# Performance work log

Hardware: AMD Instinct MI355X
Metric: run time of the kernel (lower is better)

The kernel has to match this reference:

```python
import jax, jax.numpy as jnp
import numpy as np

B, T, N1, K = 128, 512, 512, 8   # batch, steps, n_customers+1, knn_k
CAPACITY = 50.0
NEG_INF = -1e9


def setup_inputs() -> dict:
    key = jax.random.key(0)
    k0, k1, k2, k3, k4, k5 = jax.random.split(key, 6)
    psi_prime = jax.random.normal(k0, (B, N1, 2), dtype=jnp.float32)
    demands = jax.random.uniform(k1, (B, N1), dtype=jnp.float32) * 9.0 + 1.0
    demands = demands.at[:, 0].set(0.0)  # depot has zero demand
    actions = jax.random.randint(k2, (B, T), 0, N1, dtype=jnp.int32)
    knn_indices = jax.random.randint(k3, (B, N1, K), 0, N1, dtype=jnp.int32)
    Wq_w = jax.random.normal(k4, (2, 4), dtype=jnp.float32) * 0.5
    Wq_b = jax.random.normal(k5, (2,), dtype=jnp.float32) * 0.1
    lambda_param = jnp.float32(0.1)
    return {"psi_prime": psi_prime, "demands": demands, "Wq_w": Wq_w,
            "Wq_b": Wq_b, "lambda_param": lambda_param,
            "actions": actions, "knn_indices": knn_indices}


def _rollout_states(demands, actions):
    """Reconstruct the T per-step states (cur, used, vis) BEFORE each action."""
    mb, Tn = actions.shape
    n1 = demands.shape[1]
    batch = jnp.arange(mb)

    def step(carry, act_t):
        cur, used, vis = carry
        out = (cur, used, vis)  # record state before applying act_t
        at_depot = act_t == 0
        dem_t = jnp.take_along_axis(demands, act_t[:, None], axis=1)[:, 0]
        used_n = jnp.where(at_depot, 0.0, used + dem_t)
        vis_n = vis.at[batch, act_t].set(True)
        vis_n = vis_n.at[:, 0].set(False)
        return (act_t, used_n, vis_n), out

    init = (jnp.zeros((mb,), jnp.int32), jnp.zeros((mb,), jnp.float32),
            jnp.zeros((mb, n1), dtype=bool))
    _, (all_cur, all_used, all_vis) = jax.lax.scan(step, init, actions.T)
    # scan stacks over leading T axis -> move batch first
    return all_cur.T, all_used.T, jnp.transpose(all_vis, (1, 0, 2))


def _evaluate(psi_prime, demands, Wq_w, Wq_b, lambda_param, actions, knn_indices):
    mb, Tn = actions.shape
    n_cust = psi_prime.shape[1] - 1

    all_cur, all_used, all_vis = _rollout_states(demands, actions)  # [B,T],[B,T],[B,T,N1]

    remaining = CAPACITY - all_used                      # [B,T]
    cap_norm = remaining / max(CAPACITY, 1e-8)
    exceeds = demands[:, None, :] > remaining[:, :, None]  # [B,T,N1]
    mask = all_vis | exceeds
    mask = mask.at[:, :, 0].set(False)
    at_depot = all_cur == 0                               # [B,T]
    has_cust = jnp.any(~mask[:, :, 1:], axis=-1)
    mask = mask.at[:, :, 0].set(at_depot & has_cust)

    psi_curr = jnp.take_along_axis(psi_prime, all_cur[:, :, None], axis=1)  # [B,T,2]
    psi_curr = jnp.where(at_depot[:, :, None], 0.0, psi_curr)
    t_norm = jnp.arange(Tn, dtype=jnp.float32) / max(n_cust, 1)
    t_norm = jnp.broadcast_to(t_norm[None, :], (mb, Tn))
    ctx = jnp.concatenate([psi_curr, cap_norm[:, :, None], t_norm[:, :, None]], axis=-1)  # [B,T,4]

    query = ctx @ Wq_w.T + Wq_b                           # [B,T,2]
    context_scores = jnp.einsum('btd,bnd->btn', query, psi_prime)  # [B,T,N1]

    # kNN interference: per-node dot with its k nearest neighbours, summed
    neigh = psi_prime[jnp.arange(mb)[:, None, None], knn_indices]  # [B,N1,K,2]
    interf = jnp.einsum('bnd,bnkd->bn', psi_prime, neigh)          # [B,N1]

    scores = context_scores + lambda_param * interf[:, None, :]
    scores = jnp.where(mask, NEG_INF, scores)
    log_probs = jax.nn.log_softmax(scores, axis=-1)                # [B,T,N1]

    lp_new = jnp.take_along_axis(log_probs, actions[:, :, None], axis=2)[:, :, 0]  # [B,T]
    ent = -jnp.sum(jnp.exp(log_probs) * log_probs, axis=-1)        # [B,T]
    entropy = ent.mean(axis=1)                                     # [B]
    return lp_new, entropy


def reference(psi_prime, demands, Wq_w, Wq_b, lambda_param, actions, knn_indices):
    return _evaluate(psi_prime, demands, Wq_w, Wq_b, lambda_param, actions, knn_indices)
```

## Files before the change

kernel.cpp:

```cpp
#include <hip/hip_runtime.h>
#include <hip/hip_bf16.h>

#define B_  128
#define T_  512
#define N1_ 512
#define K_  8
#define CAPf 50.0f
#define NEG_INF_F (-1000000000.0f)

__device__ __forceinline__ int   fi(float x) { return __float_as_int(x); }
__device__ __forceinline__ float uf(int x)   { return __int_as_float(x); }

__device__ __forceinline__ float wave_sum64(float x) {
    x += uf(__builtin_amdgcn_update_dpp(0, fi(x), 0x111, 0xF, 0xF, true));
    x += uf(__builtin_amdgcn_update_dpp(0, fi(x), 0x112, 0xF, 0xF, true));
    x += uf(__builtin_amdgcn_update_dpp(0, fi(x), 0x114, 0xF, 0xF, true));
    x += uf(__builtin_amdgcn_update_dpp(0, fi(x), 0x118, 0xF, 0xF, true));
    x += uf(__builtin_amdgcn_update_dpp(0, fi(x), 0x142, 0xA, 0xF, true));
    x += uf(__builtin_amdgcn_update_dpp(0, fi(x), 0x143, 0xC, 0xF, true));
    return uf(__builtin_amdgcn_readlane(fi(x), 63));
}
__device__ __forceinline__ float wave_max64_pos(float x) {
    x = fmaxf(x, uf(__builtin_amdgcn_update_dpp(0, fi(x), 0x111, 0xF, 0xF, true)));
    x = fmaxf(x, uf(__builtin_amdgcn_update_dpp(0, fi(x), 0x112, 0xF, 0xF, true)));
    x = fmaxf(x, uf(__builtin_amdgcn_update_dpp(0, fi(x), 0x114, 0xF, 0xF, true)));
    x = fmaxf(x, uf(__builtin_amdgcn_update_dpp(0, fi(x), 0x118, 0xF, 0xF, true)));
    x = fmaxf(x, uf(__builtin_amdgcn_update_dpp(0, fi(x), 0x142, 0xA, 0xF, true)));
    x = fmaxf(x, uf(__builtin_amdgcn_update_dpp(0, fi(x), 0x143, 0xC, 0xF, true)));
    return uf(__builtin_amdgcn_readlane(fi(x), 63));
}

__global__ __launch_bounds__(256, 4) void fused_kernel(
    const float* __restrict__ psi,
    const float* __restrict__ demands,
    const float* __restrict__ Wq_w,
    const float* __restrict__ Wq_b,
    const float* __restrict__ lambda_p,
    const int*   __restrict__ actions,
    const int*   __restrict__ knn,
    float* __restrict__ out_lp,
    float* __restrict__ out_ent)
{
    __shared__ float4 pk_l[N1_];
    __shared__ int    fv_l[N1_];
    __shared__ int    act_l[T_];
    __shared__ float2 md_l[T_];
    __shared__ float  used_l[T_];
    __shared__ float  went[4];

    const int bid    = blockIdx.x;
    const int b      = bid >> 4;
    const int chunk  = bid & 15;
    const int t_base = chunk * 32;
    const int t_end  = t_base + 32;
    const int tid    = threadIdx.x;
    const int wave   = tid >> 6;
    const int lane   = tid & 63;

    const float2* psi2 = (const float2*)psi;
    for (int i = tid; i < N1_; i += 256) {
        float2 p = psi2[b * N1_ + i];
        pk_l[i] = make_float4(p.x, p.y, 0.0f, demands[b * N1_ + i]);
        fv_l[i] = 0x7fffffff;
    }
    for (int t = tid; t < T_; t += 256) act_l[t] = actions[b * T_ + t];
    __syncthreads();

    for (int t = tid; t < T_; t += 256) {
        int a = act_l[t];
        atomicMin(&fv_l[a], t);
        float d = pk_l[a].w;
        md_l[t] = (a == 0) ? make_float2(0.0f, 0.0f) : make_float2(1.0f, d);
    }
    const float lam = *lambda_p;
    for (int n = tid; n < N1_; n += 256) {
        float px = pk_l[n].x, py = pk_l[n].y;
        const int4* kk = (const int4*)(knn + ((size_t)b * N1_ + n) * K_);
        int4 k0 = kk[0], k1 = kk[1];
        int ks[8] = {k0.x, k0.y, k0.z, k0.w, k1.x, k1.y, k1.z, k1.w};
        float acc = 0.0f;
        #pragma unroll
        for (int k = 0; k < 8; ++k) {
            acc = fmaf(px, pk_l[ks[k]].x, acc);
            acc = fmaf(py, pk_l[ks[k]].y, acc);
        }
        pk_l[n].z = lam * acc;
    }
    __syncthreads();

    if (tid == 0) {
        float u = 0.0f;
        #pragma unroll 8
        for (int t = 0; t < t_end; ++t) {
            used_l[t] = u;
            float2 md = md_l[t];
            u = fmaf(md.x, u, md.y);
        }
    }
    float4 pk[8];
    int    fvr[8];
    #pragma unroll
    for (int j = 0; j < 8; ++j) {
        pk[j]  = pk_l[j * 64 + lane];
        fvr[j] = fv_l[j * 64 + lane];
    }
    const float W00 = Wq_w[0], W01 = Wq_w[1], W02 = Wq_w[2], W03 = Wq_w[3];
    const float W10 = Wq_w[4], W11 = Wq_w[5], W12 = Wq_w[6], W13 = Wq_w[7];
    const float bq0 = Wq_b[0], bq1 = Wq_b[1];
    __syncthreads();

    float ent_acc = 0.0f;

    #pragma unroll 1
    for (int r = 0; r < 8; ++r) {
        const int t = t_base + wave * 8 + r;

        const int   cur  = (t == 0) ? 0 : act_l[t - 1];
        const int   a    = act_l[t];
        const float rem  = CAPf - used_l[t];
        const float cap  = rem * (1.0f / CAPf);
        const float tn   = (float)t * (1.0f / 511.0f);
        const bool  at_depot = (cur == 0);

        float pcx = 0.0f, pcy = 0.0f;
        if (!at_depot) { float4 pc = pk_l[cur]; pcx = pc.x; pcy = pc.y; }

        const float q0 = fmaf(pcx, W00, fmaf(pcy, W01, fmaf(cap, W02, fmaf(tn, W03, bq0))));
        const float q1 = fmaf(pcx, W10, fmaf(pcy, W11, fmaf(cap, W12, fmaf(tn, W13, bq1))));

        float s[8];
        bool avail = false;
        #pragma unroll
        for (int j = 0; j < 8; ++j) {
            const int n = j * 64 + lane;
            float sc = fmaf(q0, pk[j].x, fmaf(q1, pk[j].y, pk[j].z));
            if (n != 0) {
                bool m = (fvr[j] < t) | (pk[j].w > rem);
                avail |= !m;
                sc = m ? NEG_INF_F : sc;
            }
            s[j] = sc;
        }

        const bool has_cust = __any((int)avail);
        if (lane == 0 && at_depot && has_cust) s[0] = NEG_INF_F;

        float pre = s[0];
        #pragma unroll
        for (int j = 1; j < 8; ++j) pre = fmaxf(pre, s[j]);
        const float mx = wave_max64_pos(pre + 1024.0f) - 1024.0f;

        float S1 = 0.0f, S2 = 0.0f;
        #pragma unroll
        for (int j = 0; j < 8; ++j) {
            float e = __expf(s[j] - mx);
            S1 += e;
            S2 = fmaf(e, s[j], S2);
        }
        S1 = wave_sum64(S1);
        S2 = wave_sum64(S2);
        const float lse = mx + __logf(S1);

        const int ja = a >> 6;
        float sv = s[0];
        sv = (ja == 1) ? s[1] : sv;
        sv = (ja == 2) ? s[2] : sv;
        sv = (ja == 3) ? s[3] : sv;
        sv = (ja == 4) ? s[4] : sv;
        sv = (ja == 5) ? s[5] : sv;
        sv = (ja == 6) ? s[6] : sv;
        sv = (ja == 7) ? s[7] : sv;
        const float s_a = uf(__builtin_amdgcn_readlane(fi(sv), a & 63));

        if (lane == 0) out_lp[b * T_ + t] = s_a - lse;
        ent_acc += lse - __fdividef(S2, S1);
    }

    if (lane == 0) went[wave] = ent_acc;
    __syncthreads();
    if (tid == 0) {
        float s = (went[0] + went[1]) + (went[2] + went[3]);
        atomicAdd(&out_ent[b], s * (1.0f / 512.0f));
    }
}

extern "C" void kernel_launch(void* const* d_in, const int* in_sizes, int n_in,
                              void* d_out, int out_size, void* d_ws, size_t ws_size,
                              hipStream_t stream) {
    const float* psi      = (const float*)d_in[0];
    const float* demands  = (const float*)d_in[1];
    const float* Wq_w     = (const float*)d_in[2];
    const float* Wq_b     = (const float*)d_in[3];
    const float* lam      = (const float*)d_in[4];
    const int*   actions  = (const int*)d_in[5];
    const int*   knn      = (const int*)d_in[6];

    float* out_lp  = (float*)d_out;
    float* out_ent = out_lp + (size_t)B_ * T_;

    fused_kernel<<<B_ * 16, 256, 0, stream>>>(psi, demands, Wq_w, Wq_b, lam,
                                              actions, knn, out_lp, out_ent);
}
```

Baseline: 99.77 us.

## Split per-batch preprocessing into separate prep kernel writing workspace

The fused kernel recomputed the per-batch setup (first-visit table, kNN interference, used-capacity scan) in each of 16 blocks per batch. This moves that setup into a prep kernel that runs once per batch and writes its results to workspace, and the main kernel then reads them from global memory. Shared memory use in the main kernel drops, so the launch bound now allows 8 blocks per multiprocessor. The cost is a second kernel launch, a global round trip, and a prep kernel with only 128 blocks whose serial scan runs in one thread.

```diff
diff --git a/kernel.cpp b/kernel.cpp
--- a/kernel.cpp
+++ b/kernel.cpp
@@ -30,79 +30,105 @@
     return uf(__builtin_amdgcn_readlane(fi(x), 63));
 }
 
-__global__ __launch_bounds__(256, 4) void fused_kernel(
+__global__ __launch_bounds__(256) void prep_kernel(
     const float* __restrict__ psi,
     const float* __restrict__ demands,
-    const float* __restrict__ Wq_w,
-    const float* __restrict__ Wq_b,
     const float* __restrict__ lambda_p,
     const int*   __restrict__ actions,
     const int*   __restrict__ knn,
+    float4* __restrict__ ws_pk,
+    int*    __restrict__ ws_fv,
+    float*  __restrict__ ws_used)
+{
+    __shared__ float2 psi_l[N1_];
+    __shared__ float  dem_l[N1_];
+    __shared__ int    fv_l[N1_];
+    __shared__ int    act_l[T_];
+    __shared__ float2 md_l[T_];
+
+    const int b   = blockIdx.x;
+    const int tid = threadIdx.x;
+
+    const float2* psi2 = (const float2*)psi;
+    for (int i = tid; i < N1_; i += 256) {
+        psi_l[i] = psi2[b * N1_ + i];
+        dem_l[i] = demands[b * N1_ + i];
+        fv_l[i]  = 0x7fffffff;
+    }
+    for (int t = tid; t < T_; t += 256) act_l[t] = actions[b * T_ + t];
+    __syncthreads();
+
+    for (int t = tid; t < T_; t += 256) {
+        int a = act_l[t];
+        atomicMin(&fv_l[a], t);
+        float d = dem_l[a];
+        md_l[t] = (a == 0) ? make_float2(0.0f, 0.0f) : make_float2(1.0f, d);
+    }
+    __syncthreads();
+
+    if (tid == 0) {
+        float u = 0.0f;
+        #pragma unroll 8
+        for (int t = 0; t < T_; ++t) {
+            ws_used[b * T_ + t] = u;
+            float2 md = md_l[t];
+            u = fmaf(md.x, u, md.y);
+        }
+    } else if (tid >= 64) {
+        const float lam = *lambda_p;
+        for (int n = tid - 64; n < N1_; n += 192) {
+            float2 p = psi_l[n];
+            const int4* kk = (const int4*)(knn + ((size_t)b * N1_ + n) * K_);
+            int4 k0 = kk[0], k1 = kk[1];
+            int ks[8] = {k0.x, k0.y, k0.z, k0.w, k1.x, k1.y, k1.z, k1.w};
+            float acc = 0.0f;
+            #pragma unroll
+            for (int k = 0; k < 8; ++k) {
+                float2 q = psi_l[ks[k]];
+                acc = fmaf(p.x, q.x, acc);
+                acc = fmaf(p.y, q.y, acc);
+            }
+            ws_pk[b * N1_ + n] = make_float4(p.x, p.y, lam * acc, dem_l[n]);
+        }
+    }
+    __syncthreads();
+    for (int n = tid; n < N1_; n += 256) ws_fv[b * N1_ + n] = fv_l[n];
+}
+
+__global__ __launch_bounds__(256, 8) void main_kernel(
+    const float*  __restrict__ Wq_w,
+    const float*  __restrict__ Wq_b,
+    const int*    __restrict__ actions,
+    const float4* __restrict__ ws_pk,
+    const int*    __restrict__ ws_fv,
+    const float*  __restrict__ ws_used,
     float* __restrict__ out_lp,
     float* __restrict__ out_ent)
 {
-    __shared__ float4 pk_l[N1_];
-    __shared__ int    fv_l[N1_];
-    __shared__ int    act_l[T_];
-    __shared__ float2 md_l[T_];
-    __shared__ float  used_l[T_];
-    __shared__ float  went[4];
+    __shared__ float used_s[32];
+    __shared__ int   act_s[33];
+    __shared__ float went[4];
 
     const int bid    = blockIdx.x;
     const int b      = bid >> 4;
     const int chunk  = bid & 15;
     const int t_base = chunk * 32;
-    const int t_end  = t_base + 32;
     const int tid    = threadIdx.x;
     const int wave   = tid >> 6;
     const int lane   = tid & 63;
 
-    const float2* psi2 = (const float2*)psi;
-    for (int i = tid; i < N1_; i += 256) {
-        float2 p = psi2[b * N1_ + i];
-        pk_l[i] = make_float4(p.x, p.y, 0.0f, demands[b * N1_ + i]);
-        fv_l[i] = 0x7fffffff;
-    }
-    for (int t = tid; t < T_; t += 256) act_l[t] = actions[b * T_ + t];
-    __syncthreads();
-
-    for (int t = tid; t < T_; t += 256) {
-        int a = act_l[t];
-        atomicMin(&fv_l[a], t);
-        float d = pk_l[a].w;
-        md_l[t] = (a == 0) ? make_float2(0.0f, 0.0f) : make_float2(1.0f, d);
-    }
-    const float lam = *lambda_p;
-    for (int n = tid; n < N1_; n += 256) {
-        float px = pk_l[n].x, py = pk_l[n].y;
-        const int4* kk = (const int4*)(knn + ((size_t)b * N1_ + n) * K_);
-        int4 k0 = kk[0], k1 = kk[1];
-        int ks[8] = {k0.x, k0.y, k0.z, k0.w, k1.x, k1.y, k1.z, k1.w};
-        float acc = 0.0f;
-        #pragma unroll
-        for (int k = 0; k < 8; ++k) {
-            acc = fmaf(px, pk_l[ks[k]].x, acc);
-            acc = fmaf(py, pk_l[ks[k]].y, acc);
-        }
-        pk_l[n].z = lam * acc;
-    }
-    __syncthreads();
-
-    if (tid == 0) {
-        float u = 0.0f;
-        #pragma unroll 8
-        for (int t = 0; t < t_end; ++t) {
-            used_l[t] = u;
-            float2 md = md_l[t];
-            u = fmaf(md.x, u, md.y);
-        }
-    }
+    if (tid < 32) used_s[tid] = ws_used[b * T_ + t_base + tid];
+    if (tid < 33) {
+        int tt = t_base - 1 + tid;
+        act_s[tid] = (tt < 0) ? 0 : actions[b * T_ + tt];
+    }
+
     float4 pk[8];
     int    fvr[8];
     #pragma unroll
     for (int j = 0; j < 8; ++j) {
-        pk[j]  = pk_l[j * 64 + lane];
-        fvr[j] = fv_l[j * 64 + lane];
+        pk[j]  = ws_pk[b * N1_ + j * 64 + lane];
+        fvr[j] = ws_fv[b * N1_ + j * 64 + lane];
     }
     const float W00 = Wq_w[0], W01 = Wq_w[1], W02 = Wq_w[2], W03 = Wq_w[3];
     const float W10 = Wq_w[4], W11 = Wq_w[5], W12 = Wq_w[6], W13 = Wq_w[7];
@@ -113,17 +139,20 @@
 
     #pragma unroll 1
     for (int r = 0; r < 8; ++r) {
-        const int t = t_base + wave * 8 + r;
-
-        const int   cur  = (t == 0) ? 0 : act_l[t - 1];
-        const int   a    = act_l[t];
-        const float rem  = CAPf - used_l[t];
-        const float cap  = rem * (1.0f / CAPf);
-        const float tn   = (float)t * (1.0f / 511.0f);
+        const int i   = wave * 8 + r;
+        const int t   = t_base + i;
+        const int cur = (t == 0) ? 0 : act_s[i];
+        const int a   = act_s[i + 1];
+        const float rem = CAPf - used_s[i];
+        const float cap = rem * (1.0f / CAPf);
+        const float tn  = (float)t * (1.0f / 511.0f);
         const bool  at_depot = (cur == 0);
 
         float pcx = 0.0f, pcy = 0.0f;
-        if (!at_depot) { float4 pc = pk_l[cur]; pcx = pc.x; pcy = pc.y; }
+        if (!at_depot) {
+            float4 pc = ws_pk[b * N1_ + cur];
+            pcx = pc.x; pcy = pc.y;
+        }
 
         const float q0 = fmaf(pcx, W00, fmaf(pcy, W01, fmaf(cap, W02, fmaf(tn, W03, bq0))));
         const float q1 = fmaf(pcx, W10, fmaf(pcy, W11, fmaf(cap, W12, fmaf(tn, W13, bq1))));
@@ -198,6 +227,13 @@
     float* out_lp  = (float*)d_out;
     float* out_ent = out_lp + (size_t)B_ * T_;
 
-    fused_kernel<<<B_ * 16, 256, 0, stream>>>(psi, demands, Wq_w, Wq_b, lam,
-                                              actions, knn, out_lp, out_ent);
-}
+    float4* ws_pk  = (float4*)d_ws;
+    int*    ws_fv  = (int*)  ((char*)d_ws + (size_t)B_ * N1_ * 16);
+    float*  ws_used= (float*)((char*)d_ws + (size_t)B_ * N1_ * 20);
+
+    prep_kernel<<<B_, 256, 0, stream>>>(psi, demands, lam, actions, knn,
+                                        ws_pk, ws_fv, ws_used);
+    main_kernel<<<B_ * 16, 256, 0, stream>>>(Wq_w, Wq_b, actions,
+                                             ws_pk, ws_fv, ws_used,
+                                             out_lp, out_ent);
+}
```

Measured after the change: 99.18 us. About the same (-0.6%).
